# Optimization experiments

Hardware: AMD Instinct MI355X
Metric: run time of the kernel (lower is better)

The kernel has to match this reference:

```python
import jax, jax.numpy as jnp
import numpy as np

T, BATCH, DMODEL, H = 2048, 16, 512, 512


def setup_inputs() -> dict:
    key = jax.random.key(0)
    ks = jax.random.split(key, 8)
    x = jax.random.normal(ks[0], (T, BATCH, DMODEL), jnp.float32)
    # initial carry: (lambda=1, h=0) so the concat trick leaves state untouched
    h0_re = jnp.zeros((1, BATCH, H), jnp.float32)
    h0_im = jnp.zeros((1, BATCH, H), jnp.float32)
    # LRU parameterization (Orvieto et al. 2023): |lambda| in [0.9, 0.99]
    u1 = jax.random.uniform(ks[1], (H,), jnp.float32)
    nu_log = jnp.log(-0.5 * jnp.log(u1 * (0.99 ** 2 - 0.9 ** 2) + 0.9 ** 2))
    theta_log = jnp.log(jax.random.uniform(ks[2], (H,), jnp.float32) * (np.pi / 10) + 1e-4)
    B_re = jax.random.normal(ks[3], (H, DMODEL), jnp.float32) / np.sqrt(2 * DMODEL)
    B_im = jax.random.normal(ks[4], (H, DMODEL), jnp.float32) / np.sqrt(2 * DMODEL)
    C_re = jax.random.normal(ks[5], (DMODEL, H), jnp.float32) / np.sqrt(H)
    C_im = jax.random.normal(ks[6], (DMODEL, H), jnp.float32) / np.sqrt(H)
    D_vec = jax.random.normal(ks[7], (DMODEL,), jnp.float32)
    return dict(x=x, h0_re=h0_re, h0_im=h0_im, nu_log=nu_log, theta_log=theta_log,
                B_re=B_re, B_im=B_im, C_re=C_re, C_im=C_im, D_vec=D_vec)


def _binop(qi, qj):
    # associative combine for h_t = a_t * h_{t-1} + b_t
    a_i, b_i = qi
    a_j, b_j = qj
    return (a_j * a_i, a_j * b_i + b_j)


def reference(x, h0_re, h0_im, nu_log, theta_log, B_re, B_im, C_re, C_im, D_vec):
    # diagonal complex recurrence eigenvalues, |Lambda| = exp(-exp(nu_log)) < 1
    Lam = jnp.exp(-jnp.exp(nu_log) + 1j * jnp.exp(theta_log))        # [H] complex64
    gamma = jnp.sqrt(1.0 - jnp.exp(-2.0 * jnp.exp(nu_log)))           # [H]
    Bmat = (B_re + 1j * B_im) * gamma[:, None]                         # [H, D]
    # map_to_h: Bu elements and broadcast Lambda elements
    Bu = jnp.einsum('tbd,hd->tbh', x.astype(jnp.complex64), Bmat)      # [T, B, H]
    Lam_el = jnp.broadcast_to(Lam, Bu.shape)                            # [T, B, H]
    # concat previous state (lambda=1, b=h0) as first scan element
    h0 = (h0_re + 1j * h0_im).astype(jnp.complex64)                    # [1, B, H]
    a = jnp.concatenate([jnp.ones_like(h0), Lam_el], axis=0)          # [T+1, B, H]
    b = jnp.concatenate([h0, Bu], axis=0)                              # [T+1, B, H]
    _, h_all = jax.lax.associative_scan(_binop, (a, b), axis=0)
    h = h_all[1:]                                                       # [T, B, H]
    # map_from_h: y = Re(C h) + D * x (elementwise skip)
    Cmat = C_re + 1j * C_im                                             # [D, H]
    y = jnp.einsum('tbh,dh->tbd', h, Cmat).real + D_vec * x            # [T, B, D]
    final_state = h[-1:]                                                # [1, B, H]
    return (final_state, y)
```

## Files before the change

kernel.cpp:

```cpp
#include <hip/hip_runtime.h>
#include <stdint.h>

typedef short shortx8 __attribute__((ext_vector_type(8)));
typedef float floatx4 __attribute__((ext_vector_type(4)));

#define T_LEN 2048
#define BATCH 16
#define DMODEL 512
#define HDIM 512
#define M_ROWS (T_LEN * BATCH)
#define NCHUNK 32
#define LCHUNK 64
#define NCHAIN (BATCH * HDIM)
#define Y_ELEMS (M_ROWS * DMODEL)

__device__ __forceinline__ unsigned short f2bf(float f) {
    union { float f; unsigned u; } v; v.f = f;
    unsigned r = (v.u + 0x7FFFu + ((v.u >> 16) & 1u)) >> 16;
    return (unsigned short)r;
}
__device__ __forceinline__ float bf2f(unsigned short u) {
    union { unsigned u; float f; } v; v.u = ((unsigned)u) << 16;
    return v.f;
}

__global__ void prep_kernel(const float* __restrict__ nu_log, const float* __restrict__ th_log,
                            float* lam_re, float* lam_im, float* l64_re, float* l64_im, float* gam) {
    int h = blockIdx.x * blockDim.x + threadIdx.x;
    if (h >= HDIM) return;
    double nu  = exp((double)nu_log[h]);
    double th  = exp((double)th_log[h]);
    double mag = exp(-nu);
    double lre = mag * cos(th), lim = mag * sin(th);
    double g   = sqrt(1.0 - exp(-2.0 * nu));
    double zr = lre, zi = lim;
    for (int i = 0; i < 6; ++i) { double nr = zr*zr - zi*zi; zi = 2.0*zr*zi; zr = nr; }
    lam_re[h] = (float)lre; lam_im[h] = (float)lim;
    l64_re[h] = (float)zr;  l64_im[h] = (float)zi;
    gam[h] = (float)g;
}

__global__ void conv_BC_kernel(const float* __restrict__ B_re, const float* __restrict__ B_im,
                               const float* __restrict__ gam,
                               const float* __restrict__ C_re, const float* __restrict__ C_im,
                               unsigned short* __restrict__ Bs, unsigned short* __restrict__ C2) {
    int idx = blockIdx.x * blockDim.x + threadIdx.x;
    if (idx < 524288) {
        int n = idx >> 9;
        int d = idx & 511;
        int h = n & 511;
        float v = (n < HDIM ? B_re[h * DMODEL + d] : B_im[h * DMODEL + d]) * gam[h];
        Bs[idx] = f2bf(v);
    } else {
        int i2 = idx - 524288;
        int d = i2 >> 10;
        int k = i2 & 1023;
        float v = (k < HDIM) ? C_re[d * HDIM + k] : -C_im[d * HDIM + (k - HDIM)];
        C2[i2] = f2bf(v);
    }
}

__global__ void cast_x_kernel(const float4* __restrict__ x4, unsigned short* __restrict__ xb, int n4) {
    int i = blockIdx.x * blockDim.x + threadIdx.x;
    if (i >= n4) return;
    float4 v = x4[i];
    ushort4 u;
    u.x = f2bf(v.x); u.y = f2bf(v.y); u.z = f2bf(v.z); u.w = f2bf(v.w);
    *(ushort4*)(xb + (size_t)i * 4) = u;
}

template <int MODE>
__global__ __launch_bounds__(256) void gemm_nt(const unsigned short* __restrict__ A,
                                               const unsigned short* __restrict__ Bmat,
                                               const int K, const int N, const int lgNB,
                                               unsigned short* __restrict__ OutB,
                                               float* __restrict__ OutF,
                                               const float* __restrict__ Dv,
                                               const float* __restrict__ Xf) {
    __shared__ unsigned short As[128 * 32];
    __shared__ unsigned short Bs[128 * 32];
    const int L = blockIdx.x;
    const int xcd = L & 7;
    const int slot = L >> 3;
    const int bn = slot & ((1 << lgNB) - 1);
    const int bm = xcd * 32 + (slot >> lgNB);
    const int tid = threadIdx.x;
    const int wv = tid >> 6, lane = tid & 63;
    const int wr = wv >> 1, wc = wv & 1;
    const int lrow = lane & 15, qq = lane >> 4;
    floatx4 acc[4][4] = {};

    const size_t rowA = (size_t)bm * 128, rowB = (size_t)bn * 128;
    for (int k0 = 0; k0 < K; k0 += 32) {
        #pragma unroll
        for (int j = 0; j < 2; ++j) {
            int chunk = j * 256 + wv * 64 + lane;
            int r  = chunk >> 2;
            int cc = (chunk & 3) * 8;
            const unsigned short* ga = A    + (rowA + r) * (size_t)K + (k0 + cc);
            const unsigned short* gb = Bmat + (rowB + r) * (size_t)K + (k0 + cc);
            unsigned short* la = As + (size_t)(j * 256 + wv * 64) * 8;
            unsigned short* lb = Bs + (size_t)(j * 256 + wv * 64) * 8;
            __builtin_amdgcn_global_load_lds((const __attribute__((address_space(1))) void*)ga,
                                             (__attribute__((address_space(3))) void*)la, 16, 0, 0);
            __builtin_amdgcn_global_load_lds((const __attribute__((address_space(1))) void*)gb,
                                             (__attribute__((address_space(3))) void*)lb, 16, 0, 0);
        }
        __syncthreads();
        shortx8 af[4], bf[4];
        #pragma unroll
        for (int mi = 0; mi < 4; ++mi)
            af[mi] = *(const shortx8*)&As[(wr * 64 + mi * 16 + lrow) * 32 + qq * 8];
        #pragma unroll
        for (int ni = 0; ni < 4; ++ni)
            bf[ni] = *(const shortx8*)&Bs[(wc * 64 + ni * 16 + lrow) * 32 + qq * 8];
        #pragma unroll
        for (int mi = 0; mi < 4; ++mi)
            #pragma unroll
            for (int ni = 0; ni < 4; ++ni)
                acc[mi][ni] = __builtin_amdgcn_mfma_f32_16x16x32_bf16(af[mi], bf[ni], acc[mi][ni], 0, 0, 0);
        __syncthreads();
    }

    #pragma unroll
    for (int mi = 0; mi < 4; ++mi) {
        int mbase = bm * 128 + wr * 64 + mi * 16 + qq * 4;
        #pragma unroll
        for (int ni = 0; ni < 4; ++ni) {
            int n = bn * 128 + wc * 64 + ni * 16 + lrow;
            if (MODE == 0) {
                #pragma unroll
                for (int r = 0; r < 4; ++r)
                    OutB[(size_t)(mbase + r) * N + n] = f2bf(acc[mi][ni][r]);
            } else {
                float dv = Dv[n];
                #pragma unroll
                for (int r = 0; r < 4; ++r) {
                    size_t idx = (size_t)(mbase + r) * N + n;
                    OutF[idx] = acc[mi][ni][r] + dv * Xf[idx];
                }
            }
        }
    }
}

__global__ void scan_partial(const unsigned short* __restrict__ Bu,
                             const float* __restrict__ lam_re, const float* __restrict__ lam_im,
                             float* __restrict__ car_re, float* __restrict__ car_im) {
    int gid = blockIdx.x * blockDim.x + threadIdx.x;
    int chunk = gid >> 12;
    int idx = gid & 4095;
    int b = idx >> 8, hp = idx & 255;
    int h = hp * 2;
    float lr0 = lam_re[h], li0 = lam_im[h];
    float lr1 = lam_re[h + 1], li1 = lam_im[h + 1];
    float v0r = 0.f, v0i = 0.f, v1r = 0.f, v1i = 0.f;
    const unsigned short* p = Bu + (size_t)chunk * LCHUNK * BATCH * 1024 + (size_t)b * 1024 + h;
    for (int j = 0; j < LCHUNK; ++j) {
        unsigned rr = *(const unsigned*)p;
        unsigned ii = *(const unsigned*)(p + 512);
        float b0r = bf2f((unsigned short)rr), b1r = bf2f((unsigned short)(rr >> 16));
        float b0i = bf2f((unsigned short)ii), b1i = bf2f((unsigned short)(ii >> 16));
        float n0r = lr0 * v0r - li0 * v0i + b0r;
        float n0i = lr0 * v0i + li0 * v0r + b0i;
        float n1r = lr1 * v1r - li1 * v1i + b1r;
        float n1i = lr1 * v1i + li1 * v1r + b1i;
        v0r = n0r; v0i = n0i; v1r = n1r; v1i = n1i;
        p += BATCH * 1024;
    }
    int c = b * 512 + h;
    *(float2*)&car_re[chunk * NCHAIN + c] = make_float2(v0r, v1r);
    *(float2*)&car_im[chunk * NCHAIN + c] = make_float2(v0i, v1i);
}

__global__ void scan_combine(const float* __restrict__ car_re, const float* __restrict__ car_im,
                             const float* __restrict__ l64_re, const float* __restrict__ l64_im,
                             const float* __restrict__ h0_re, const float* __restrict__ h0_im,
                             float* __restrict__ cin_re, float* __restrict__ cin_im,
                             float* __restrict__ out_final, int interleave) {
    int c = blockIdx.x * blockDim.x + threadIdx.x;
    int h = c & 511;
    float lre = l64_re[h], lim = l64_im[h];
    float vre = h0_re[c], vim = h0_im[c];
    for (int k = 0; k < NCHUNK; ++k) {
        cin_re[k * NCHAIN + c] = vre;
        cin_im[k * NCHAIN + c] = vim;
        float cr = car_re[k * NCHAIN + c], ci = car_im[k * NCHAIN + c];
        float nr = lre * vre - lim * vim + cr;
        float ni = lre * vim + lim * vre + ci;
        vre = nr; vim = ni;
    }
    if (interleave) {
        out_final[2 * c]     = vre;
        out_final[2 * c + 1] = vim;
    } else {
        out_final[c] = vre;
    }
}

__global__ void scan_apply(unsigned short* __restrict__ Bu,
                           const float* __restrict__ lam_re, const float* __restrict__ lam_im,
                           const float* __restrict__ cin_re, const float* __restrict__ cin_im) {
    int gid = blockIdx.x * blockDim.x + threadIdx.x;
    int chunk = gid >> 12;
    int idx = gid & 4095;
    int b = idx >> 8, hp = idx & 255;
    int h = hp * 2;
    int c = b * 512 + h;
    float lr0 = lam_re[h], li0 = lam_im[h];
    float lr1 = lam_re[h + 1], li1 = lam_im[h + 1];
    float2 cr = *(const float2*)&cin_re[chunk * NCHAIN + c];
    float2 ci = *(const float2*)&cin_im[chunk * NCHAIN + c];
    float v0r = cr.x, v0i = ci.x, v1r = cr.y, v1i = ci.y;
    unsigned short* p = Bu + (size_t)chunk * LCHUNK * BATCH * 1024 + (size_t)b * 1024 + h;
    for (int j = 0; j < LCHUNK; ++j) {
        unsigned rr = *(const unsigned*)p;
        unsigned ii = *(const unsigned*)(p + 512);
        float b0r = bf2f((unsigned short)rr), b1r = bf2f((unsigned short)(rr >> 16));
        float b0i = bf2f((unsigned short)ii), b1i = bf2f((unsigned short)(ii >> 16));
        float n0r = lr0 * v0r - li0 * v0i + b0r;
        float n0i = lr0 * v0i + li0 * v0r + b0i;
        float n1r = lr1 * v1r - li1 * v1i + b1r;
        float n1i = lr1 * v1i + li1 * v1r + b1i;
        v0r = n0r; v0i = n0i; v1r = n1r; v1i = n1i;
        *(unsigned*)p         = (unsigned)f2bf(v0r) | ((unsigned)f2bf(v1r) << 16);
        *(unsigned*)(p + 512) = (unsigned)f2bf(v0i) | ((unsigned)f2bf(v1i) << 16);
        p += BATCH * 1024;
    }
}

extern "C" void kernel_launch(void* const* d_in, const int* in_sizes, int n_in,
                              void* d_out, int out_size, void* d_ws, size_t ws_size,
                              hipStream_t stream) {
    const float* x        = (const float*)d_in[0];
    const float* h0_re    = (const float*)d_in[1];
    const float* h0_im    = (const float*)d_in[2];
    const float* nu_log   = (const float*)d_in[3];
    const float* theta_lg = (const float*)d_in[4];
    const float* B_re     = (const float*)d_in[5];
    const float* B_im     = (const float*)d_in[6];
    const float* C_re     = (const float*)d_in[7];
    const float* C_im     = (const float*)d_in[8];
    const float* D_vec    = (const float*)d_in[9];

    char* ws = (char*)d_ws;
    unsigned short* BuH  = (unsigned short*)(ws + 0);
    unsigned short* xb   = (unsigned short*)(ws + 67108864);
    unsigned short* Bs   = (unsigned short*)(ws + 100663296);
    unsigned short* C2   = (unsigned short*)(ws + 101711872);
    float* car_re        = (float*)(ws + 102760448);
    float* car_im        = (float*)(ws + 103809024);
    float* cin_re        = (float*)(ws + 104857600);
    float* cin_im        = (float*)(ws + 105906176);
    float* lam_re        = (float*)(ws + 106954752);
    float* lam_im        = (float*)(ws + 106956800);
    float* l64_re        = (float*)(ws + 106958848);
    float* l64_im        = (float*)(ws + 106960896);
    float* gam           = (float*)(ws + 106962944);

    int fs_elems = out_size - Y_ELEMS;
    int interleave = (fs_elems == 8192) ? 0 : 1;
    if (fs_elems != 8192) fs_elems = 16384;
    float* out_final = (float*)d_out;
    float* y_out     = (float*)d_out + fs_elems;

    prep_kernel<<<2, 256, 0, stream>>>(nu_log, theta_lg, lam_re, lam_im, l64_re, l64_im, gam);
    conv_BC_kernel<<<(1048576) / 256, 256, 0, stream>>>(B_re, B_im, gam, C_re, C_im, Bs, C2);
    cast_x_kernel<<<(Y_ELEMS / 4) / 256, 256, 0, stream>>>((const float4*)x, xb, Y_ELEMS / 4);
    gemm_nt<0><<<2048, 256, 0, stream>>>(xb, Bs, DMODEL, 1024, 3, BuH, nullptr, nullptr, nullptr);
    scan_partial<<<(NCHUNK * NCHAIN / 2) / 256, 256, 0, stream>>>(BuH, lam_re, lam_im, car_re, car_im);
    scan_combine<<<NCHAIN / 256, 256, 0, stream>>>(car_re, car_im, l64_re, l64_im,
                                                   h0_re, h0_im, cin_re, cin_im, out_final, interleave);
    scan_apply<<<(NCHUNK * NCHAIN / 2) / 256, 256, 0, stream>>>(BuH, lam_re, lam_im, cin_re, cin_im);
    gemm_nt<1><<<1024, 256, 0, stream>>>(BuH, C2, 1024, 512, 2, nullptr, y_out, D_vec, x);
}
```

Before: 291.0 us.

## Swizzle GEMM LDS with K=64 tiles, fuse scan combine into apply

The GEMM now stages 64-wide K tiles with an XOR swizzle on LDS columns to avoid bank conflicts and halve barrier count, and requests higher occupancy. The separate scan_combine kernel is removed; each scan_apply thread recomputes its chunk's carry-in by iterating over prior chunk carries, saving a launch and the cin buffers at the cost of redundant work. The output epilogue reads the bf16 copy of x instead of fp32 x, cutting bandwidth but reducing precision of the D*x skip term.

After: 259.4 us. 10.9% less time.

```diff
diff --git a/kernel.cpp b/kernel.cpp
--- a/kernel.cpp
+++ b/kernel.cpp
@@ -70,15 +70,15 @@
 }
 
 template <int MODE>
-__global__ __launch_bounds__(256) void gemm_nt(const unsigned short* __restrict__ A,
-                                               const unsigned short* __restrict__ Bmat,
-                                               const int K, const int N, const int lgNB,
-                                               unsigned short* __restrict__ OutB,
-                                               float* __restrict__ OutF,
-                                               const float* __restrict__ Dv,
-                                               const float* __restrict__ Xf) {
-    __shared__ unsigned short As[128 * 32];
-    __shared__ unsigned short Bs[128 * 32];
+__global__ __launch_bounds__(256, 4) void gemm_nt(const unsigned short* __restrict__ A,
+                                                  const unsigned short* __restrict__ Bmat,
+                                                  const int K, const int N, const int lgNB,
+                                                  unsigned short* __restrict__ OutB,
+                                                  float* __restrict__ OutF,
+                                                  const float* __restrict__ Dv,
+                                                  const unsigned short* __restrict__ Xb) {
+    __shared__ unsigned short As[128 * 64];
+    __shared__ unsigned short Bs[128 * 64];
     const int L = blockIdx.x;
     const int xcd = L & 7;
     const int slot = L >> 3;
@@ -91,14 +91,15 @@
     floatx4 acc[4][4] = {};
 
     const size_t rowA = (size_t)bm * 128, rowB = (size_t)bn * 128;
-    for (int k0 = 0; k0 < K; k0 += 32) {
+    for (int k0 = 0; k0 < K; k0 += 64) {
         #pragma unroll
-        for (int j = 0; j < 2; ++j) {
-            int chunk = j * 256 + wv * 64 + lane;
-            int r  = chunk >> 2;
-            int cc = (chunk & 3) * 8;
-            const unsigned short* ga = A    + (rowA + r) * (size_t)K + (k0 + cc);
-            const unsigned short* gb = Bmat + (rowB + r) * (size_t)K + (k0 + cc);
+        for (int j = 0; j < 4; ++j) {
+            int ch  = j * 256 + wv * 64 + lane;
+            int r   = ch >> 3;
+            int c16 = ch & 7;
+            int g16 = c16 ^ (r & 7);
+            const unsigned short* ga = A    + (rowA + r) * (size_t)K + (k0 + g16 * 8);
+            const unsigned short* gb = Bmat + (rowB + r) * (size_t)K + (k0 + g16 * 8);
             unsigned short* la = As + (size_t)(j * 256 + wv * 64) * 8;
             unsigned short* lb = Bs + (size_t)(j * 256 + wv * 64) * 8;
             __builtin_amdgcn_global_load_lds((const __attribute__((address_space(1))) void*)ga,
@@ -107,18 +108,27 @@
                                              (__attribute__((address_space(3))) void*)lb, 16, 0, 0);
         }
         __syncthreads();
-        shortx8 af[4], bf[4];
         #pragma unroll
-        for (int mi = 0; mi < 4; ++mi)
-            af[mi] = *(const shortx8*)&As[(wr * 64 + mi * 16 + lrow) * 32 + qq * 8];
-        #pragma unroll
-        for (int ni = 0; ni < 4; ++ni)
-            bf[ni] = *(const shortx8*)&Bs[(wc * 64 + ni * 16 + lrow) * 32 + qq * 8];
-        #pragma unroll
-        for (int mi = 0; mi < 4; ++mi)
+        for (int s = 0; s < 2; ++s) {
+            shortx8 af[4], bf[4];
             #pragma unroll
-            for (int ni = 0; ni < 4; ++ni)
-                acc[mi][ni] = __builtin_amdgcn_mfma_f32_16x16x32_bf16(af[mi], bf[ni], acc[mi][ni], 0, 0, 0);
+            for (int mi = 0; mi < 4; ++mi) {
+                int row = wr * 64 + mi * 16 + lrow;
+                int c16 = (s * 4 + qq) ^ (row & 7);
+                af[mi] = *(const shortx8*)&As[row * 64 + c16 * 8];
+            }
+            #pragma unroll
+            for (int ni = 0; ni < 4; ++ni) {
+                int row = wc * 64 + ni * 16 + lrow;
+                int c16 = (s * 4 + qq) ^ (row & 7);
+                bf[ni] = *(const shortx8*)&Bs[row * 64 + c16 * 8];
+            }
+            #pragma unroll
+            for (int mi = 0; mi < 4; ++mi)
+                #pragma unroll
+                for (int ni = 0; ni < 4; ++ni)
+                    acc[mi][ni] = __builtin_amdgcn_mfma_f32_16x16x32_bf16(af[mi], bf[ni], acc[mi][ni], 0, 0, 0);
+        }
         __syncthreads();
     }
 
@@ -137,7 +147,7 @@
                 #pragma unroll
                 for (int r = 0; r < 4; ++r) {
                     size_t idx = (size_t)(mbase + r) * N + n;
-                    OutF[idx] = acc[mi][ni][r] + dv * Xf[idx];
+                    OutF[idx] = acc[mi][ni][r] + dv * bf2f(Xb[idx]);
                 }
             }
         }
@@ -173,45 +183,33 @@
     *(float2*)&car_im[chunk * NCHAIN + c] = make_float2(v0i, v1i);
 }
 
-__global__ void scan_combine(const float* __restrict__ car_re, const float* __restrict__ car_im,
-                             const float* __restrict__ l64_re, const float* __restrict__ l64_im,
-                             const float* __restrict__ h0_re, const float* __restrict__ h0_im,
-                             float* __restrict__ cin_re, float* __restrict__ cin_im,
-                             float* __restrict__ out_final, int interleave) {
-    int c = blockIdx.x * blockDim.x + threadIdx.x;
-    int h = c & 511;
-    float lre = l64_re[h], lim = l64_im[h];
-    float vre = h0_re[c], vim = h0_im[c];
-    for (int k = 0; k < NCHUNK; ++k) {
-        cin_re[k * NCHAIN + c] = vre;
-        cin_im[k * NCHAIN + c] = vim;
-        float cr = car_re[k * NCHAIN + c], ci = car_im[k * NCHAIN + c];
-        float nr = lre * vre - lim * vim + cr;
-        float ni = lre * vim + lim * vre + ci;
-        vre = nr; vim = ni;
-    }
-    if (interleave) {
-        out_final[2 * c]     = vre;
-        out_final[2 * c + 1] = vim;
-    } else {
-        out_final[c] = vre;
-    }
-}
-
 __global__ void scan_apply(unsigned short* __restrict__ Bu,
                            const float* __restrict__ lam_re, const float* __restrict__ lam_im,
-                           const float* __restrict__ cin_re, const float* __restrict__ cin_im) {
+                           const float* __restrict__ l64_re, const float* __restrict__ l64_im,
+                           const float* __restrict__ h0_re, const float* __restrict__ h0_im,
+                           const float* __restrict__ car_re, const float* __restrict__ car_im,
+                           float* __restrict__ out_final, int interleave) {
     int gid = blockIdx.x * blockDim.x + threadIdx.x;
     int chunk = gid >> 12;
     int idx = gid & 4095;
     int b = idx >> 8, hp = idx & 255;
     int h = hp * 2;
     int c = b * 512 + h;
+    float L0r = l64_re[h], L0i = l64_im[h];
+    float L1r = l64_re[h + 1], L1i = l64_im[h + 1];
+    float v0r = h0_re[c], v0i = h0_im[c];
+    float v1r = h0_re[c + 1], v1i = h0_im[c + 1];
+    for (int k = 0; k < chunk; ++k) {
+        float2 crr = *(const float2*)&car_re[k * NCHAIN + c];
+        float2 cii = *(const float2*)&car_im[k * NCHAIN + c];
+        float n0r = L0r * v0r - L0i * v0i + crr.x;
+        float n0i = L0r * v0i + L0i * v0r + cii.x;
+        float n1r = L1r * v1r - L1i * v1i + crr.y;
+        float n1i = L1r * v1i + L1i * v1r + cii.y;
+        v0r = n0r; v0i = n0i; v1r = n1r; v1i = n1i;
+    }
     float lr0 = lam_re[h], li0 = lam_im[h];
     float lr1 = lam_re[h + 1], li1 = lam_im[h + 1];
-    float2 cr = *(const float2*)&cin_re[chunk * NCHAIN + c];
-    float2 ci = *(const float2*)&cin_im[chunk * NCHAIN + c];
-    float v0r = cr.x, v0i = ci.x, v1r = cr.y, v1i = ci.y;
     unsigned short* p = Bu + (size_t)chunk * LCHUNK * BATCH * 1024 + (size_t)b * 1024 + h;
     for (int j = 0; j < LCHUNK; ++j) {
         unsigned rr = *(const unsigned*)p;
@@ -227,6 +225,17 @@
         *(unsigned*)(p + 512) = (unsigned)f2bf(v0i) | ((unsigned)f2bf(v1i) << 16);
         p += BATCH * 1024;
     }
+    if (chunk == NCHUNK - 1) {
+        if (interleave) {
+            out_final[2 * c]     = v0r;
+            out_final[2 * c + 1] = v0i;
+            out_final[2 * c + 2] = v1r;
+            out_final[2 * c + 3] = v1i;
+        } else {
+            out_final[c]     = v0r;
+            out_final[c + 1] = v1r;
+        }
+    }
 }
 
 extern "C" void kernel_launch(void* const* d_in, const int* in_sizes, int n_in,
@@ -250,13 +259,11 @@
     unsigned short* C2   = (unsigned short*)(ws + 101711872);
     float* car_re        = (float*)(ws + 102760448);
     float* car_im        = (float*)(ws + 103809024);
-    float* cin_re        = (float*)(ws + 104857600);
-    float* cin_im        = (float*)(ws + 105906176);
-    float* lam_re        = (float*)(ws + 106954752);
-    float* lam_im        = (float*)(ws + 106956800);
-    float* l64_re        = (float*)(ws + 106958848);
-    float* l64_im        = (float*)(ws + 106960896);
-    float* gam           = (float*)(ws + 106962944);
+    float* lam_re        = (float*)(ws + 104857600);
+    float* lam_im        = (float*)(ws + 104859648);
+    float* l64_re        = (float*)(ws + 104861696);
+    float* l64_im        = (float*)(ws + 104863744);
+    float* gam           = (float*)(ws + 104865792);
 
     int fs_elems = out_size - Y_ELEMS;
     int interleave = (fs_elems == 8192) ? 0 : 1;
@@ -269,8 +276,8 @@
     cast_x_kernel<<<(Y_ELEMS / 4) / 256, 256, 0, stream>>>((const float4*)x, xb, Y_ELEMS / 4);
     gemm_nt<0><<<2048, 256, 0, stream>>>(xb, Bs, DMODEL, 1024, 3, BuH, nullptr, nullptr, nullptr);
     scan_partial<<<(NCHUNK * NCHAIN / 2) / 256, 256, 0, stream>>>(BuH, lam_re, lam_im, car_re, car_im);
-    scan_combine<<<NCHAIN / 256, 256, 0, stream>>>(car_re, car_im, l64_re, l64_im,
-                                                   h0_re, h0_im, cin_re, cin_im, out_final, interleave);
-    scan_apply<<<(NCHUNK * NCHAIN / 2) / 256, 256, 0, stream>>>(BuH, lam_re, lam_im, cin_re, cin_im);
-    gemm_nt<1><<<1024, 256, 0, stream>>>(BuH, C2, 1024, 512, 2, nullptr, y_out, D_vec, x);
-}
+    scan_apply<<<(NCHUNK * NCHAIN / 2) / 256, 256, 0, stream>>>(BuH, lam_re, lam_im, l64_re, l64_im,
+                                                                h0_re, h0_im, car_re, car_im,
+                                                                out_final, interleave);
+    gemm_nt<1><<<1024, 256, 0, stream>>>(BuH, C2, 1024, 512, 2, nullptr, y_out, D_vec, xb);
+}
```
